# Kernel tuning notes

Measured on AMD Instinct MI355X. Metric: run time of the kernel, lower is better.

Reference implementation:

```python
import jax, jax.numpy as jnp
import numpy as np
from jax import lax

B, H, W, C, K, R, CB = 2, 128, 128, 256, 64, 8, 256


def _conv(x, w, b=None, pad=1, lhs_dil=None, groups=1):
    out = lax.conv_general_dilated(x, w, (1, 1), [(pad, pad), (pad, pad)],
                                   lhs_dilation=lhs_dil, feature_group_count=groups,
                                   dimension_numbers=('NCHW', 'OIHW', 'NCHW'))
    return out if b is None else out + b[None, :, None, None]


def _silu(x):
    return x * jax.nn.sigmoid(x)


def _fuse(l0, l1, l2, p1w, p1b, p2w, p3w):
    # proj1: Conv(k=3)+SiLU (BN folded); proj2/proj3: grouped ConvTranspose2d as lhs-dilated grouped convs
    a = _silu(_conv(l0, p1w, p1b))
    b2 = _conv(l1, p2w, pad=2, lhs_dil=(2, 2), groups=CB)  # ConvT(2CB->CB, k4, s2, p1, g=CB)
    b3 = _conv(l2, p3w, pad=5, lhs_dil=(4, 4), groups=CB)  # ConvT(4CB->CB, k8, s4, p2, g=CB)
    return a + b2 + b3


def _corr_map(emb, trk):
    # emb: [H,W,C], trk: [K,C]; cosine-similarity correlation with local argmax radius masking
    e = emb / jnp.maximum(jnp.linalg.norm(emb, axis=-1, keepdims=True), 1e-12)
    t = trk / jnp.maximum(jnp.linalg.norm(trk, axis=-1, keepdims=True), 1e-12)
    y = jnp.maximum(jnp.einsum('hwc,kc->khw', e, t), 0.0)  # torch.where(y>0, y, 0)
    idx = jnp.argmax(y.reshape(K, -1), axis=1)             # first max, like torch.nonzero(...)[0]
    ai, aj = idx // W, idx % W
    rows = jnp.arange(H)[None, :, None]
    cols = jnp.arange(W)[None, None, :]
    m = ((rows >= (ai[:, None, None] - R)) & (rows < (ai[:, None, None] + R)) &
         (cols >= (aj[:, None, None] - R)) & (cols < (aj[:, None, None] + R)))
    s = jnp.sum(y * m, axis=0)
    return s / jnp.max(s)


def setup_inputs():
    key = jax.random.key(0)
    ks = jax.random.split(key, 32)
    r = lambda i, shp, s=0.02: jax.random.normal(ks[i], shp, jnp.float32) * s
    z = lambda n: jnp.zeros((n,), jnp.float32)
    return dict(
        id_embeding=jax.random.normal(ks[0], (B, H, W, C), jnp.float32),
        tracklets=jax.random.normal(ks[1], (B, K, C), jnp.float32),
        l0=jax.random.normal(ks[2], (B, CB, H, W), jnp.float32),
        l1=jax.random.normal(ks[3], (B, 2 * CB, H // 2, W // 2), jnp.float32),
        l2=jax.random.normal(ks[4], (B, 4 * CB, H // 4, W // 4), jnp.float32),
        b_p1w=r(5, (CB, CB, 3, 3)), b_p1b=z(CB),
        b_p2w=r(6, (CB, 2, 4, 4)), b_p3w=r(7, (CB, 4, 8, 8)),
        b_c1w=r(8, (CB, CB, 3, 3)), b_c1b=z(CB),
        b_c2w=r(9, (4, CB, 3, 3)), b_c2b=z(4),
        h_p1w=r(10, (CB, CB, 3, 3)), h_p1b=z(CB),
        h_p2w=r(11, (CB, 2, 4, 4)), h_p3w=r(12, (CB, 4, 8, 8)),
        h_c1aw=r(13, (CB, 1, 3, 3), 0.1), h_c1ab=z(CB),
        h_c1bw=r(14, (1, CB, 3, 3)), h_c1bb=z(1),
        h_c2aw=r(15, (CB, CB, 3, 3)), h_c2ab=z(CB),
        h_c2bw=r(16, (CB, CB, 3, 3)), h_c2bb=z(CB),
        h_c2cw=r(17, (1, CB, 3, 3)), h_c2cb=z(1),
    )


def reference(id_embeding, tracklets, l0, l1, l2,
              b_p1w, b_p1b, b_p2w, b_p3w, b_c1w, b_c1b, b_c2w, b_c2b,
              h_p1w, h_p1b, h_p2w, h_p3w,
              h_c1aw, h_c1ab, h_c1bw, h_c1bb,
              h_c2aw, h_c2ab, h_c2bw, h_c2bb, h_c2cw, h_c2cb):
    # correlation map per batch -> x_F [B,1,H,W]
    x_F = jax.vmap(_corr_map)(id_embeding, tracklets)[:, None]
    # recheck_Box head
    xd_box = _fuse(l0, l1, l2, b_p1w, b_p1b, b_p2w, b_p3w)
    xb = _silu(_conv(xd_box, b_c1w, b_c1b))
    siambox = jnp.transpose(_conv(xb, b_c2w, b_c2b), (0, 2, 3, 1))  # [B,H,W,4]
    # recheck_heatmap head
    xd_hm = _fuse(l0, l1, l2, h_p1w, h_p1b, h_p2w, h_p3w)
    xf = _conv(_silu(_conv(x_F, h_c1aw, h_c1ab)), h_c1bw, h_c1bb)   # [B,1,H,W]
    t = xf * xd_hm                                                  # broadcast over CB channels
    t = _silu(_conv(t, h_c2aw, h_c2ab))
    t = _silu(_conv(t, h_c2bw, h_c2bb))
    hmmap = jax.nn.sigmoid(_conv(t, h_c2cw, h_c2cb))                # [B,1,H,W]
    return (hmmap, siambox)
```

## Files before the change

kernel.cpp:

```cpp
#include <hip/hip_runtime.h>
#include <math.h>

#define HH 128
#define WW 128
#define HWSZ 16384
#define CC 256
#define KK 64
#define BB 2

typedef __bf16 bf16x8_t __attribute__((ext_vector_type(8)));
typedef float  f32x4_t  __attribute__((ext_vector_type(4)));

__device__ __forceinline__ float silu_f(float v) { return v / (1.f + expf(-v)); }
__device__ __forceinline__ float sigm_f(float v) { return 1.f / (1.f + expf(-v)); }

__device__ __forceinline__ float b2f(unsigned short u) {
    union { unsigned int i; float f; } x; x.i = ((unsigned int)u) << 16; return x.f;
}
__device__ __forceinline__ unsigned short f2b(float f) {
    union { float f; unsigned int i; } x; x.f = f;
    unsigned int r = x.i + 0x7FFFu + ((x.i >> 16) & 1u);
    return (unsigned short)(r >> 16);
}
__device__ __forceinline__ float u2f(unsigned int u) {
    union { unsigned int i; float f; } x; x.i = u; return x.f;
}

__device__ __forceinline__ void cvt_nhwc_body(int bid, float (*T)[128],
                                              const float* __restrict__ in,
                                              unsigned short* __restrict__ out,
                                              unsigned long long* __restrict__ ymax,
                                              unsigned int* __restrict__ umax) {
    const int tid = threadIdx.x;
    if (bid == 0) {
        if (tid < BB * KK) ymax[tid] = 0ull;
        if (tid >= 128 && tid < 128 + BB) umax[tid - 128] = 0u;
    }
    const int y = bid & 127;
    const int b = bid >> 7;
    const float* inb = in + (size_t)b * CC * HWSZ + y * 128;
    unsigned short* outb = out + ((size_t)b * HWSZ + (size_t)y * 128) * CC;

    for (int c0 = 0; c0 < CC; c0 += 32) {
        __syncthreads();
        {
            int cl = tid >> 3;
            int xq = tid & 7;
            const float4* src = (const float4*)(inb + (size_t)(c0 + cl) * HWSZ);
            float4* dst = (float4*)&T[cl][0];
            #pragma unroll
            for (int j = 0; j < 4; j++) dst[xq * 4 + j] = src[xq * 4 + j];
        }
        __syncthreads();
        {
            int x = tid & 127, ch = tid >> 7;
            union { unsigned short u[16]; uint4 v[2]; } pk;
            #pragma unroll
            for (int j = 0; j < 16; j++) pk.u[j] = f2b(T[ch * 16 + j][x]);
            uint4* dst = (uint4*)&outb[(size_t)x * CC + c0 + ch * 16];
            dst[0] = pk.v[0];
            dst[1] = pk.v[1];
        }
    }
}

#define WTSZ (9 * 8 * 256 * 32)
__device__ __forceinline__ void wprep_body(int L,
                                           const float* const* ws,
                                           unsigned short* __restrict__ wtbase) {
    int set = L / 2304;
    int blk = L - set * 2304;
    const float* w = ws[set];
    int idx = blk * 256 + threadIdx.x;
    int e   = idx & 7;
    int co  = (idx >> 3) & 255;
    int g   = (idx >> 11) & 3;
    int v   = idx >> 13;
    int cb  = v / 9;
    int t   = v - cb * 9;
    wtbase[(size_t)set * WTSZ + idx] = f2b(w[((size_t)co * 256 + cb * 32 + g * 8 + e) * 9 + t]);
}

__global__ __launch_bounds__(256) void prep_fused_kernel(
    const float* __restrict__ l0, unsigned short* __restrict__ l0nh,
    unsigned long long* __restrict__ ymax, unsigned int* __restrict__ umax,
    const float* __restrict__ w0, const float* __restrict__ w1,
    const float* __restrict__ w2, const float* __restrict__ w3,
    const float* __restrict__ w4, unsigned short* __restrict__ wtbase)
{
    __shared__ float T[32][128];
    const int bid = blockIdx.x;
    if (bid < 256) {
        cvt_nhwc_body(bid, T, l0, l0nh, ymax, umax);
    } else {
        const float* ws[5] = {w0, w1, w2, w3, w4};
        wprep_body(bid - 256, ws, wtbase);
    }
}

#define EPAD 260
__global__ __launch_bounds__(256) void ycorr_kernel(const float* __restrict__ emb,
                                                    const float* __restrict__ trk,
                                                    float* __restrict__ y,
                                                    unsigned long long* __restrict__ ymax) {
    __shared__ __align__(16) float E[64 * EPAD];
    __shared__ __align__(16) float T[64 * EPAD];
    __shared__ float SE[64];
    __shared__ float ST[64];

    const int tid = threadIdx.x;
    const int b   = blockIdx.y;
    const int hw0 = blockIdx.x * 64;

    const float4* esrc = (const float4*)(emb + ((size_t)b * HWSZ + hw0) * CC);
    #pragma unroll
    for (int i = 0; i < 16; i++) {
        int q  = tid + i * 256;
        int px = q >> 6, c4 = q & 63;
        *(float4*)&E[px * EPAD + c4 * 4] = esrc[(size_t)px * 64 + c4];
    }
    const float4* tsrc = (const float4*)(trk + (size_t)b * KK * CC);
    #pragma unroll
    for (int i = 0; i < 16; i++) {
        int q = tid + i * 256;
        int k = q >> 6, c4 = q & 63;
        *(float4*)&T[k * EPAD + c4 * 4] = tsrc[(size_t)k * 64 + c4];
    }
    __syncthreads();

    if (tid < 64) {
        float ss = 0.f;
        const float4* ep = (const float4*)&E[tid * EPAD];
        #pragma unroll 8
        for (int c4 = 0; c4 < 64; c4++) {
            float4 v = ep[c4];
            ss += v.x * v.x + v.y * v.y + v.z * v.z + v.w * v.w;
        }
        SE[tid] = 1.f / fmaxf(sqrtf(ss), 1e-12f);
    } else if (tid < 128) {
        float ss = 0.f;
        const float4* tp = (const float4*)&T[(tid - 64) * EPAD];
        #pragma unroll 8
        for (int c4 = 0; c4 < 64; c4++) {
            float4 v = tp[c4];
            ss += v.x * v.x + v.y * v.y + v.z * v.z + v.w * v.w;
        }
        ST[tid - 64] = 1.f / fmaxf(sqrtf(ss), 1e-12f);
    }
    __syncthreads();

    const int pg = tid & 15;
    const int kg = tid >> 4;

    float acc[4][4];
    #pragma unroll
    for (int jp = 0; jp < 4; jp++)
        #pragma unroll
        for (int jk = 0; jk < 4; jk++) acc[jp][jk] = 0.f;

    const float* Ep[4];
    const float* Tp[4];
    #pragma unroll
    for (int jp = 0; jp < 4; jp++) Ep[jp] = &E[(jp * 16 + pg) * EPAD];
    #pragma unroll
    for (int jk = 0; jk < 4; jk++) Tp[jk] = &T[(jk * 16 + kg) * EPAD];

    #pragma unroll 2
    for (int c4 = 0; c4 < 64; ++c4) {
        float4 e[4], t[4];
        #pragma unroll
        for (int jp = 0; jp < 4; jp++) e[jp] = *(const float4*)(Ep[jp] + c4 * 4);
        #pragma unroll
        for (int jk = 0; jk < 4; jk++) t[jk] = *(const float4*)(Tp[jk] + c4 * 4);
        #define DOT4(a, t) (fmaf(a.w, t.w, fmaf(a.z, t.z, fmaf(a.y, t.y, a.x * t.x))))
        #pragma unroll
        for (int jp = 0; jp < 4; jp++)
            #pragma unroll
            for (int jk = 0; jk < 4; jk++)
                acc[jp][jk] += DOT4(e[jp], t[jk]);
        #undef DOT4
    }

    #pragma unroll
    for (int jk = 0; jk < 4; jk++) {
        int k = jk * 16 + kg;
        float st = ST[k];
        unsigned long long best = 0ull;
        #pragma unroll
        for (int jp = 0; jp < 4; jp++) {
            int px = jp * 16 + pg;
            float val = fmaxf(acc[jp][jk], 0.f) * SE[px] * st;
            y[((size_t)b * KK + k) * HWSZ + hw0 + px] = val;
            union { float f; unsigned int i; } u; u.f = val;
            unsigned long long pk =
                ((unsigned long long)u.i << 32) | (unsigned)(HWSZ - 1 - (hw0 + px));
            best = best > pk ? best : pk;
        }
        #pragma unroll
        for (int m = 1; m < 16; m <<= 1) {
            unsigned long long o = __shfl_xor(best, m);
            best = best > o ? best : o;
        }
        if (pg == 0) atomicMax(&ymax[b * KK + k], best);
    }
}

__device__ __forceinline__ void smap_body(int bid, char* smem,
                                          const float* __restrict__ y,
                                          const unsigned long long* __restrict__ ymax,
                                          float* __restrict__ s,
                                          unsigned int* __restrict__ umax) {
    int* ai = (int*)smem;
    int* aj = (int*)(smem + 256);
    float* sm = (float*)(smem + 512);

    int b  = bid >> 6;
    int hw = (bid & 63) * 256 + threadIdx.x;
    int h  = hw >> 7, w = hw & 127;
    if (threadIdx.x < KK) {
        unsigned long long p = ymax[b * KK + threadIdx.x];
        int v = HWSZ - 1 - (int)(p & 0xFFFFFFFFull);
        ai[threadIdx.x] = v >> 7;
        aj[threadIdx.x] = v & 127;
    }
    __syncthreads();
    const float* yb = y + (size_t)b * KK * HWSZ;
    float acc = 0.f;
    #pragma unroll 8
    for (int k = 0; k < KK; k++) {
        float v = yb[(size_t)k * HWSZ + hw];
        bool in = (h >= ai[k] - 8) && (h < ai[k] + 8) && (w >= aj[k] - 8) && (w < aj[k] + 8);
        acc += in ? v : 0.f;
    }
    s[(size_t)b * HWSZ + hw] = acc;

    sm[threadIdx.x] = acc;
    __syncthreads();
    for (int st = 128; st > 0; st >>= 1) {
        if (threadIdx.x < st) sm[threadIdx.x] = fmaxf(sm[threadIdx.x], sm[threadIdx.x + st]);
        __syncthreads();
    }
    if (threadIdx.x == 0) {
        union { float f; unsigned int i; } x; x.f = sm[0];
        atomicMax(&umax[b], x.i);
    }
}

template <int HEADS>
__device__ __forceinline__ void deconv_body(int bid, char* smem,
                                            const float* __restrict__ l1,
                                            const float* __restrict__ l2,
                                            const float* __restrict__ w2a,
                                            const float* __restrict__ w3a,
                                            const float* __restrict__ w2b,
                                            const float* __restrict__ w3b,
                                            unsigned short* __restrict__ outA,
                                            unsigned short* __restrict__ outB) {
    float (*L1)[64][64] = (float (*)[64][64])smem;
    float (*L2)[32][32] = (float (*)[32][32])(smem + 32768);

    const int tid = threadIdx.x;
    const int g   = bid & 255;
    const int b   = bid >> 8;

    const float4* l1b = (const float4*)(l1 + ((size_t)b * 2 * CC + 2 * g) * 4096);
    float4* L1p = (float4*)&L1[0][0][0];
    #pragma unroll
    for (int i = 0; i < 8; i++) L1p[tid + i * 256] = l1b[tid + i * 256];
    const float4* l2b = (const float4*)(l2 + ((size_t)b * 4 * CC + 4 * g) * 1024);
    float4* L2p = (float4*)&L2[0][0][0];
    #pragma unroll
    for (int i = 0; i < 4; i++) L2p[tid + i * 256] = l2b[tid + i * 256];

    const int x    = tid & 127;
    const int ytop = tid >> 7;

    const int pxo = x & 1, pyo = ytop & 1;
    const int mx0 = (x + pxo - 2) >> 1;
    const int dy2 = (ytop + pyo - 2) >> 1;
    const bool nok0 = (unsigned)mx0 < 64u;
    const bool nok1 = (unsigned)(mx0 + 1) < 64u;
    const int nc0 = mx0 & 63, nc1 = (mx0 + 1) & 63;

    const int px3 = (5 - (x & 3)) & 3;
    const int n30 = (x + px3 - 5) >> 2;
    const bool n3ok0 = (unsigned)n30 < 32u;
    const bool n3ok1 = (unsigned)(n30 + 1) < 32u;
    const int n3c0 = n30 & 31, n3c1 = (n30 + 1) & 31;
    int dy3[2], py3v[2];
    #pragma unroll
    for (int ph = 0; ph < 2; ph++) {
        int py3 = (5 - ((ytop + 2 * ph) & 3)) & 3;
        py3v[ph] = py3;
        dy3[ph] = (2 * ph + ytop + py3 - 5) >> 2;
    }

    __syncthreads();

    const float* w2s[2] = {w2a, w2b};
    const float* w3s[2] = {w3a, w3b};
    unsigned short* outs[2] = {outA, outB};

    #pragma unroll 1
    for (int hd = 0; hd < HEADS; ++hd) {
        const float* w2g = w2s[hd] + (size_t)g * 32;
        const float* w3g = w3s[hd] + (size_t)g * 256;

        float W2[2][2][2];
        #pragma unroll
        for (int ci = 0; ci < 2; ci++)
            #pragma unroll
            for (int a = 0; a < 2; a++)
                #pragma unroll
                for (int c = 0; c < 2; c++)
                    W2[ci][a][c] = w2g[ci * 16 + (pyo + 2 * a) * 4 + (pxo + 2 * c)];
        float W3[2][4][2][2];
        #pragma unroll
        for (int ph = 0; ph < 2; ph++)
            #pragma unroll
            for (int ci = 0; ci < 4; ci++)
                #pragma unroll
                for (int a = 0; a < 2; a++)
                    #pragma unroll
                    for (int c = 0; c < 2; c++)
                        W3[ph][ci][a][c] = w3g[ci * 64 + (py3v[ph] + 4 * a) * 8 + (px3 + 4 * c)];

        unsigned short* outb = outs[hd] + ((size_t)b * CC + g) * HWSZ;

        #pragma unroll 2
        for (int ii = 0; ii < 32; ++ii) {
            #pragma unroll
            for (int ph = 0; ph < 2; ph++) {
                const int i = 2 * ii + ph;
                float acc = 0.f;
                {
                    const int m0 = i + dy2;
                    #pragma unroll
                    for (int a = 0; a < 2; a++) {
                        int m = m0 + a;
                        bool mok = (unsigned)m < 64u;
                        int mc = m & 63;
                        #pragma unroll
                        for (int ci = 0; ci < 2; ci++) {
                            float v0 = (mok && nok0) ? L1[ci][mc][nc0] : 0.f;
                            float v1 = (mok && nok1) ? L1[ci][mc][nc1] : 0.f;
                            acc = fmaf(W2[ci][a][0], v0, acc);
                            acc = fmaf(W2[ci][a][1], v1, acc);
                        }
                    }
                }
                {
                    const int m0 = ii + dy3[ph];
                    #pragma unroll
                    for (int a = 0; a < 2; a++) {
                        int m = m0 + a;
                        bool mok = (unsigned)m < 32u;
                        int mc = m & 31;
                        #pragma unroll
                        for (int ci = 0; ci < 4; ci++) {
                            float v0 = (mok && n3ok0) ? L2[ci][mc][n3c0] : 0.f;
                            float v1 = (mok && n3ok1) ? L2[ci][mc][n3c1] : 0.f;
                            acc = fmaf(W3[ph][ci][a][0], v0, acc);
                            acc = fmaf(W3[ph][ci][a][1], v1, acc);
                        }
                    }
                }
                outb[(size_t)i * 256 + tid] = f2b(acc);
            }
        }
    }
}

__global__ __launch_bounds__(256) void smap_kernel(const float* __restrict__ y,
                                                   const unsigned long long* __restrict__ ymax,
                                                   float* __restrict__ s,
                                                   unsigned int* __restrict__ umax) {
    __shared__ __align__(16) char smem[1536];
    smap_body(blockIdx.x, smem, y, ymax, s, umax);
}
template <int HEADS>
__global__ __launch_bounds__(256) void deconv_kernel(const float* __restrict__ l1,
                                                     const float* __restrict__ l2,
                                                     const float* __restrict__ w2a,
                                                     const float* __restrict__ w3a,
                                                     const float* __restrict__ w2b,
                                                     const float* __restrict__ w3b,
                                                     unsigned short* __restrict__ outA,
                                                     unsigned short* __restrict__ outB) {
    __shared__ __align__(16) char smem[49152];
    deconv_body<HEADS>(blockIdx.x, smem, l1, l2, w2a, w3a, w2b, w3b, outA, outB);
}

__global__ __launch_bounds__(256) void smapdeconv_kernel(
    const float* __restrict__ y, const unsigned long long* __restrict__ ymax,
    float* __restrict__ s, unsigned int* __restrict__ umax,
    const float* __restrict__ l1, const float* __restrict__ l2,
    const float* __restrict__ w2a, const float* __restrict__ w3a,
    const float* __restrict__ w2b, const float* __restrict__ w3b,
    unsigned short* __restrict__ outA, unsigned short* __restrict__ outB)
{
    __shared__ __align__(16) char smem[49152];
    const int bid = blockIdx.x;
    if (bid < 128) smap_body(bid, smem, y, ymax, s, umax);
    else           deconv_body<2>(bid - 128, smem, l1, l2, w2a, w3a, w2b, w3b, outA, outB);
}

template <int ADDB, int MULF>
__device__ __forceinline__ void conv_mfma_body(
    int y0, int co0, int b,
    const unsigned short* __restrict__ in,
    const unsigned short* __restrict__ wt,
    const float* __restrict__ bias,
    const unsigned short* __restrict__ addb,
    const float* __restrict__ xf,
    unsigned short* __restrict__ out,
    unsigned short (*Alds)[3 * 130 * 32])
{
    const int tid  = threadIdx.x;
    const int lane = tid & 63;
    const int wv   = tid >> 6;
    const int wco  = wv >> 1;
    const int wpx  = wv & 1;
    const int l15  = lane & 15;
    const int kg   = lane >> 4;

    const unsigned short* inb = in + (size_t)b * HWSZ * CC;
    const float* xfb = MULF ? (xf + (size_t)b * HWSZ) : nullptr;
    const unsigned short* wp = wt + (size_t)kg * 2048 + (size_t)(co0 + wco * 64 + l15) * 8;

    int ach[3][4];
    #pragma unroll
    for (int tl = 0; tl < 3; tl++)
        #pragma unroll
        for (int f = 0; f < 4; f++) {
            int px = wpx * 64 + f * 16 + l15 + tl;
            ach[tl][f] = (px * 4 + (kg ^ ((px >> 1) & 3))) * 8;
        }

    f32x4_t acc[4][4];
    #pragma unroll
    for (int i = 0; i < 4; i++)
        #pragma unroll
        for (int j = 0; j < 4; j++)
            acc[i][j] = (f32x4_t){0.f, 0.f, 0.f, 0.f};

    if (tid < 48) {
        int q4 = tid & 3;
        int hp = (tid >> 2) & 1;
        int r  = (tid >> 3) % 3;
        int bi = tid / 24;
        int px = hp ? 129 : 0;
        int chunk = (r * 130 + px) * 4 + (q4 ^ ((px >> 1) & 3));
        *reinterpret_cast<uint4*>(&Alds[bi][chunk * 8]) = make_uint4(0u, 0u, 0u, 0u);
    }

    uint4 streg[6];
    float sxf[6];

    auto load_A = [&](int cb) {
        #pragma unroll
        for (int i = 0; i < 6; i++) {
            int q   = tid + i * 256;
            int q4  = q & 3;
            int pxi = (q >> 2) & 127;
            int r   = q >> 9;
            int gy  = y0 - 1 + r;
            uint4 v = make_uint4(0u, 0u, 0u, 0u);
            float fxv = 0.f;
            if ((unsigned)gy < 128u) {
                v = *reinterpret_cast<const uint4*>(
                        inb + ((size_t)(gy * 128 + pxi)) * CC + cb * 32 + q4 * 8);
                if (MULF) fxv = xfb[gy * 128 + pxi];
            }
            streg[i] = v;
            if (MULF) sxf[i] = fxv;
        }
    };
    auto write_A = [&](int bufi) {
        #pragma unroll
        for (int i = 0; i < 6; i++) {
            int q   = tid + i * 256;
            int q4  = q & 3;
            int pxi = (q >> 2) & 127;
            int r   = q >> 9;
            int px  = pxi + 1;
            int chunk = (r * 130 + px) * 4 + (q4 ^ ((px >> 1) & 3));
            uint4 v = streg[i];
            if (MULF) {
                union { unsigned short u[8]; uint4 w; } pk;
                pk.w = v;
                float fm = sxf[i];
                #pragma unroll
                for (int e = 0; e < 8; e++) pk.u[e] = f2b(b2f(pk.u[e]) * fm);
                v = pk.w;
            }
            *reinterpret_cast<uint4*>(&Alds[bufi][chunk * 8]) = v;
        }
    };

    load_A(0);
    write_A(0);

    bf16x8_t W[3][4], P[2][4];
    #pragma unroll
    for (int f = 0; f < 4; f++) W[0][f] = *reinterpret_cast<const bf16x8_t*>(wp + f * 128);
    #pragma unroll
    for (int f = 0; f < 4; f++) W[1][f] = *reinterpret_cast<const bf16x8_t*>(wp + 8192 + f * 128);

    __syncthreads();
    #pragma unroll
    for (int f = 0; f < 4; f++)
        P[0][f] = *reinterpret_cast<const bf16x8_t*>(&Alds[0][ach[0][f]]);

    for (int cb = 0; cb < 8; ++cb) {
        const int bufi = cb & 1;
        if (cb + 1 < 8) load_A(cb + 1);
        const unsigned short* wcb = wp + (size_t)cb * 73728;
        #pragma unroll
        for (int t = 0; t < 9; ++t) {
            if (cb < 7 || t < 7) {
                #pragma unroll
                for (int f = 0; f < 4; f++)
                    W[(t + 2) % 3][f] = *reinterpret_cast<const bf16x8_t*>(
                        wcb + (t + 2) * 8192 + f * 128);
            }
            if (t < 8) {
                const int aoff = ((t + 1) / 3) * 4160;
                #pragma unroll
                for (int f = 0; f < 4; f++)
                    P[(t + 1) & 1][f] = *reinterpret_cast<const bf16x8_t*>(
                        &Alds[bufi][aoff + ach[(t + 1) % 3][f]]);
            }
            __builtin_amdgcn_sched_barrier(0);
            #pragma unroll
            for (int cf = 0; cf < 4; cf++)
                #pragma unroll
                for (int pf = 0; pf < 4; pf++)
                    acc[cf][pf] = __builtin_amdgcn_mfma_f32_16x16x32_bf16(
                        W[t % 3][cf], P[t & 1][pf], acc[cf][pf], 0, 0, 0);
        }
        if (cb + 1 < 8) write_A(bufi ^ 1);
        __syncthreads();
        if (cb + 1 < 8) {
            #pragma unroll
            for (int f = 0; f < 4; f++)
                P[0][f] = *reinterpret_cast<const bf16x8_t*>(&Alds[(cb + 1) & 1][ach[0][f]]);
        }
    }

    size_t outB = ((size_t)b * HWSZ + (size_t)y0 * 128) * CC;
    #pragma unroll
    for (int cf = 0; cf < 4; cf++) {
        int co = co0 + wco * 64 + cf * 16 + kg * 4;
        float bs0 = bias[co], bs1 = bias[co + 1], bs2 = bias[co + 2], bs3 = bias[co + 3];
        #pragma unroll
        for (int pf = 0; pf < 4; pf++) {
            int x = wpx * 64 + pf * 16 + l15;
            float v0 = silu_f(acc[cf][pf][0] + bs0);
            float v1 = silu_f(acc[cf][pf][1] + bs1);
            float v2 = silu_f(acc[cf][pf][2] + bs2);
            float v3 = silu_f(acc[cf][pf][3] + bs3);
            if (ADDB) {
                size_t ab = ((size_t)b * CC + co) * HWSZ + (size_t)y0 * 128 + x;
                v0 += b2f(addb[ab]);
                v1 += b2f(addb[ab + HWSZ]);
                v2 += b2f(addb[ab + 2 * HWSZ]);
                v3 += b2f(addb[ab + 3 * HWSZ]);
            }
            union { unsigned short u[4]; uint2 v; } pk;
            pk.u[0] = f2b(v0); pk.u[1] = f2b(v1); pk.u[2] = f2b(v2); pk.u[3] = f2b(v3);
            *reinterpret_cast<uint2*>(&out[outB + (size_t)x * CC + co]) = pk.v;
        }
    }
}

template <int ADDB, int MULF>
__global__ __launch_bounds__(256, 2) void conv_mfma_kernel(
    const unsigned short* __restrict__ in,
    const unsigned short* __restrict__ wt,
    const float* __restrict__ bias,
    const unsigned short* __restrict__ addb,
    const float* __restrict__ xf,
    unsigned short* __restrict__ out)
{
    __shared__ __align__(16) unsigned short Alds[2][3 * 130 * 32];
    const int l   = (blockIdx.x & 7) * 64 + (blockIdx.x >> 3);
    const int y0  = l >> 2;
    const int co0 = ((l >> 1) & 1) * 128;
    const int b   = l & 1;
    conv_mfma_body<ADDB, MULF>(y0, co0, b, in, wt, bias, addb, xf, out, Alds);
}

__global__ __launch_bounds__(256, 2) void conv_mfma_dual_kernel(
    const unsigned short* __restrict__ in,
    const unsigned short* __restrict__ wt2set,
    const float* __restrict__ biasB,
    const float* __restrict__ biasH,
    const unsigned short* __restrict__ addbB,
    const unsigned short* __restrict__ addbH,
    unsigned short* __restrict__ outB,
    unsigned short* __restrict__ outH)
{
    __shared__ __align__(16) unsigned short Alds[2][3 * 130 * 32];
    const int l    = (blockIdx.x & 7) * 128 + (blockIdx.x >> 3);
    const int y0   = l >> 3;
    const int c3   = l & 7;
    const int head = c3 >> 2;
    const int co0  = ((c3 >> 1) & 1) * 128;
    const int b    = c3 & 1;
    conv_mfma_body<1, 0>(y0, co0, b, in, wt2set + (size_t)head * WTSZ,
                         head ? biasH : biasB, head ? addbH : addbB,
                         nullptr, head ? outH : outB, Alds);
}

__global__ __launch_bounds__(256, 2) void conv_mfma_dualmix_kernel(
    const unsigned short* __restrict__ in0,
    const unsigned short* __restrict__ in1,
    const unsigned short* __restrict__ wt0,
    const unsigned short* __restrict__ wt1,
    const float* __restrict__ bias0,
    const float* __restrict__ bias1,
    const float* __restrict__ xf,
    unsigned short* __restrict__ out0,
    unsigned short* __restrict__ out1)
{
    __shared__ __align__(16) unsigned short Alds[2][3 * 130 * 32];
    const int l    = (blockIdx.x & 7) * 128 + (blockIdx.x >> 3);
    const int y0   = l >> 3;
    const int c3   = l & 7;
    const int head = c3 >> 2;
    const int co0  = ((c3 >> 1) & 1) * 128;
    const int b    = c3 & 1;
    if (head == 0)
        conv_mfma_body<0, 0>(y0, co0, b, in0, wt0, bias0, nullptr, nullptr, out0, Alds);
    else
        conv_mfma_body<0, 1>(y0, co0, b, in1, wt1, bias1, nullptr, xf, out1, Alds);
}

__global__ __launch_bounds__(256) void conv_c1a_kernel(const float* __restrict__ s,
                                                       const unsigned int* __restrict__ umax,
                                                       const float* __restrict__ w,
                                                       const float* __restrict__ bias,
                                                       unsigned short* __restrict__ out) {
    __shared__ float W[2304];
    __shared__ float S[3][34];

    const int tid = threadIdx.x;
    const int idx = blockIdx.x;
    const int b   = idx >> 9;
    const int seg = idx & 511;
    const int y   = seg >> 2;
    const int x0  = (seg & 3) * 32;

    for (int i = tid; i < 2304; i += 256) W[i] = w[i];
    if (tid < 102) {
        int r = tid / 34, xx = tid - r * 34;
        int gy = y - 1 + r, gx = x0 - 1 + xx;
        S[r][xx] = ((unsigned)gy < 128u && (unsigned)gx < 128u)
                       ? s[(size_t)b * HWSZ + gy * 128 + gx] : 0.f;
    }
    __syncthreads();

    const float im = 1.f / u2f(umax[b]);
    const int cog = tid >> 5;
    const int px  = tid & 31;

    float sv[9];
    #pragma unroll
    for (int r = 0; r < 3; r++)
        #pragma unroll
        for (int d = 0; d < 3; d++)
            sv[r * 3 + d] = S[r][px + d];

    unsigned short* op =
        &out[((size_t)b * HWSZ + (size_t)y * 128 + x0 + px) * CC + cog * 32];
    #pragma unroll
    for (int q = 0; q < 4; q++) {
        union { unsigned short u[8]; uint4 v; } pk;
        #pragma unroll
        for (int j = 0; j < 8; j++) {
            int co = cog * 32 + q * 8 + j;
            float a = 0.f;
            #pragma unroll
            for (int t = 0; t < 9; t++) a = fmaf(W[co * 9 + t], sv[t], a);
            pk.u[j] = f2b(silu_f(a * im + bias[co]));
        }
        *reinterpret_cast<uint4*>(op + q * 8) = pk.v;
    }
}

template <int COUT, int MODE>
__device__ __forceinline__ void small_conv_body(int bid, float* WL,
                                                const unsigned short* __restrict__ in,
                                                const float* __restrict__ w,
                                                const float* __restrict__ bias,
                                                float* __restrict__ out)
{
    const int tid = threadIdx.x;
    for (int i = tid; i < COUT * 2304; i += 256) {
        int e = i & 7;
        int g = (i >> 3) & 31;
        int rest = i >> 8;
        int t = rest % 9;
        int co = rest / 9;
        WL[((co * 9 + t) * 32 + g) * 12 + e] = w[((size_t)co * 256 + g * 8 + e) * 9 + t];
    }
    __syncthreads();

    const int lane = tid & 63;
    const int wv   = tid >> 6;
    const int c32  = lane & 31;
    const int ps   = lane >> 5;
    const int grp  = bid * 4 + wv;
    const int base = grp * 4;
    const int b    = base >> 14;
    const int pix  = base & (HWSZ - 1);
    const int y    = pix >> 7;
    const int x0   = pix & 127;
    const int p0x  = x0 + 2 * ps;

    const unsigned short* inb = in + (size_t)b * HWSZ * CC;

    uint4 d[3][4];
    #pragma unroll
    for (int r = 0; r < 3; r++) {
        int gy = y - 1 + r;
        #pragma unroll
        for (int cx = 0; cx < 4; cx++) {
            int gx = p0x - 1 + cx;
            uint4 v = make_uint4(0u, 0u, 0u, 0u);
            if ((unsigned)gy < 128u && (unsigned)gx < 128u)
                v = *reinterpret_cast<const uint4*>(
                        inb + ((size_t)(gy * 128 + gx)) * CC + c32 * 8);
            d[r][cx] = v;
        }
    }

    float acc[2][COUT];
    #pragma unroll
    for (int p = 0; p < 2; p++)
        #pragma unroll
        for (int c = 0; c < COUT; c++) acc[p][c] = 0.f;

    #pragma unroll
    for (int r = 0; r < 3; r++) {
        float f[4][8];
        #pragma unroll
        for (int cx = 0; cx < 4; cx++) {
            union { unsigned short u[8]; uint4 v; } pk;
            pk.v = d[r][cx];
            #pragma unroll
            for (int e = 0; e < 8; e++) f[cx][e] = b2f(pk.u[e]);
        }
        #pragma unroll
        for (int dx = 0; dx < 3; dx++) {
            #pragma unroll
            for (int co = 0; co < COUT; co++) {
                int bse = ((co * 9 + r * 3 + dx) * 32 + c32) * 12;
                float4 wa = *(const float4*)&WL[bse];
                float4 wb = *(const float4*)&WL[bse + 4];
                #pragma unroll
                for (int p = 0; p < 2; p++) {
                    const float* ff = f[dx + p];
                    float a = acc[p][co];
                    a = fmaf(ff[0], wa.x, a); a = fmaf(ff[1], wa.y, a);
                    a = fmaf(ff[2], wa.z, a); a = fmaf(ff[3], wa.w, a);
                    a = fmaf(ff[4], wb.x, a); a = fmaf(ff[5], wb.y, a);
                    a = fmaf(ff[6], wb.z, a); a = fmaf(ff[7], wb.w, a);
                    acc[p][co] = a;
                }
            }
        }
    }

    #pragma unroll
    for (int m = 1; m <= 16; m <<= 1)
        #pragma unroll
        for (int p = 0; p < 2; p++)
            #pragma unroll
            for (int co = 0; co < COUT; co++)
                acc[p][co] += __shfl_xor(acc[p][co], m);

    if (c32 == 0) {
        #pragma unroll
        for (int p = 0; p < 2; p++) {
            size_t pixidx = (size_t)base + 2 * ps + p;
            if (MODE == 0) {
                ((float4*)out)[pixidx] = make_float4(
                    acc[p][0] + bias[0],
                    acc[p][COUT > 1 ? 1 : 0] + bias[COUT > 1 ? 1 : 0],
                    acc[p][COUT > 2 ? 2 : 0] + bias[COUT > 2 ? 2 : 0],
                    acc[p][COUT > 3 ? 3 : 0] + bias[COUT > 3 ? 3 : 0]);
            } else if (MODE == 1) {
                out[pixidx] = acc[p][0] + bias[0];
            } else {
                out[pixidx] = sigm_f(acc[p][0] + bias[0]);
            }
        }
    }
}

template <int COUT, int MODE>
__global__ __launch_bounds__(256) void small_conv_kernel(
    const unsigned short* __restrict__ in,
    const float* __restrict__ w,
    const float* __restrict__ bias,
    float* __restrict__ out)
{
    __shared__ float WL[COUT * 9 * 32 * 12];
    small_conv_body<COUT, MODE>(blockIdx.x, WL, in, w, bias, out);
}

__global__ __launch_bounds__(256, 2) void t3c2_kernel(
    const unsigned short* __restrict__ t2in,
    const unsigned short* __restrict__ wt4,
    const float* __restrict__ biasT3,
    unsigned short* __restrict__ t3out,
    const unsigned short* __restrict__ xbin,
    const float* __restrict__ c2w,
    const float* __restrict__ c2b,
    float* __restrict__ boxout)
{
    __shared__ __align__(16) char smem[55296];
    const int bid = blockIdx.x;
    if (bid < 512) {
        const int l   = (bid & 7) * 64 + (bid >> 3);
        const int y0  = l >> 2;
        const int co0 = ((l >> 1) & 1) * 128;
        const int b   = l & 1;
        conv_mfma_body<0, 0>(y0, co0, b, t2in, wt4, biasT3, nullptr, nullptr, t3out,
                             (unsigned short (*)[3 * 130 * 32])smem);
    } else {
        small_conv_body<4, 0>(bid - 512, (float*)smem, xbin, c2w, c2b, boxout);
    }
}

extern "C" void kernel_launch(void* const* d_in, const int* in_sizes, int n_in,
                              void* d_out, int out_size, void* d_ws, size_t ws_size,
                              hipStream_t stream) {
    const float* emb    = (const float*)d_in[0];
    const float* trk    = (const float*)d_in[1];
    const float* l0     = (const float*)d_in[2];
    const float* l1     = (const float*)d_in[3];
    const float* l2     = (const float*)d_in[4];
    const float* b_p1w  = (const float*)d_in[5];
    const float* b_p1b  = (const float*)d_in[6];
    const float* b_p2w  = (const float*)d_in[7];
    const float* b_p3w  = (const float*)d_in[8];
    const float* b_c1w  = (const float*)d_in[9];
    const float* b_c1b  = (const float*)d_in[10];
    const float* b_c2w  = (const float*)d_in[11];
    const float* b_c2b  = (const float*)d_in[12];
    const float* h_p1w  = (const float*)d_in[13];
    const float* h_p1b  = (const float*)d_in[14];
    const float* h_p2w  = (const float*)d_in[15];
    const float* h_p3w  = (const float*)d_in[16];
    const float* h_c1aw = (const float*)d_in[17];
    const float* h_c1ab = (const float*)d_in[18];
    const float* h_c1bw = (const float*)d_in[19];
    const float* h_c1bb = (const float*)d_in[20];
    const float* h_c2aw = (const float*)d_in[21];
    const float* h_c2ab = (const float*)d_in[22];
    const float* h_c2bw = (const float*)d_in[23];
    const float* h_c2bb = (const float*)d_in[24];
    const float* h_c2cw = (const float*)d_in[25];
    const float* h_c2cb = (const float*)d_in[26];

    float* outp = (float*)d_out;

    const size_t ACT = (size_t)BB * CC * HWSZ;
    const size_t WT  = (size_t)WTSZ;
    const size_t SMALLS = 132096;

    unsigned short* l0nh = (unsigned short*)d_ws;
    unsigned short* wtP  = l0nh + ACT;
    unsigned short* bufA = wtP + 5 * WT;
    unsigned short* bufB = bufA + ACT;
    unsigned short* bufC = bufB + ACT;
    float* sbuf   = (float*)(bufC + ACT);
    float* xfb    = sbuf + (size_t)BB * HWSZ;
    unsigned long long* ymax = (unsigned long long*)(xfb + (size_t)BB * HWSZ);
    unsigned int* umax = (unsigned int*)(ymax + BB * KK);
    unsigned short* bufD = bufC + ACT + SMALLS;
    float* ybuf   = (float*)bufB;

    const size_t NEED = (size_t)(bufD + ACT - l0nh) * sizeof(unsigned short);
    const bool fast = ws_size >= NEED;

    prep_fused_kernel<<<256 + 11520, 256, 0, stream>>>(
        l0, l0nh, ymax, umax, b_p1w, h_p1w, b_c1w, h_c2aw, h_c2bw, wtP);

    ycorr_kernel<<<dim3(256, BB), 256, 0, stream>>>(emb, trk, ybuf, ymax);

    if (fast) {
        smapdeconv_kernel<<<128 + 512, 256, 0, stream>>>(
            ybuf, ymax, sbuf, umax,
            l1, l2, b_p2w, b_p3w, h_p2w, h_p3w, bufA, bufD);
        conv_c1a_kernel<<<1024, 256, 0, stream>>>(sbuf, umax, h_c1aw, h_c1ab, bufB);
        small_conv_kernel<1, 1><<<2048, 256, 0, stream>>>(bufB, h_c1bw, h_c1bb, xfb);
        conv_mfma_dual_kernel<<<1024, 256, 0, stream>>>(l0nh, wtP, b_p1b, h_p1b,
                                                        bufA, bufD, bufB, bufC);
        conv_mfma_dualmix_kernel<<<1024, 256, 0, stream>>>(bufB, bufC,
                                                           wtP + 2 * WT, wtP + 3 * WT,
                                                           b_c1b, h_c2ab, xfb,
                                                           bufD, bufA);
        t3c2_kernel<<<512 + 2048, 256, 0, stream>>>(bufA, wtP + 4 * WT, h_c2bb, bufB,
                                                    bufD, b_c2w, b_c2b,
                                                    outp + BB * HWSZ);
        small_conv_kernel<1, 2><<<2048, 256, 0, stream>>>(bufB, h_c2cw, h_c2cb, outp);
    } else {
        smap_kernel<<<64 * BB, 256, 0, stream>>>(ybuf, ymax, sbuf, umax);
        deconv_kernel<1><<<BB * CC, 256, 0, stream>>>(l1, l2, b_p2w, b_p3w,
                                                      nullptr, nullptr, bufA, nullptr);
        conv_mfma_kernel<1, 0><<<512, 256, 0, stream>>>(l0nh, wtP, b_p1b, bufA,
                                                        nullptr, bufB);
        conv_mfma_kernel<0, 0><<<512, 256, 0, stream>>>(bufB, wtP + 2 * WT, b_c1b,
                                                        nullptr, nullptr, bufC);
        small_conv_kernel<4, 0><<<2048, 256, 0, stream>>>(bufC, b_c2w, b_c2b,
                                                          outp + BB * HWSZ);
        deconv_kernel<1><<<BB * CC, 256, 0, stream>>>(l1, l2, h_p2w, h_p3w,
                                                      nullptr, nullptr, bufA, nullptr);
        conv_mfma_kernel<1, 0><<<512, 256, 0, stream>>>(l0nh, wtP + 1 * WT, h_p1b, bufA,
                                                        nullptr, bufB);
        conv_c1a_kernel<<<1024, 256, 0, stream>>>(sbuf, umax, h_c1aw, h_c1ab, bufC);
        small_conv_kernel<1, 1><<<2048, 256, 0, stream>>>(bufC, h_c1bw, h_c1bb, xfb);
        conv_mfma_kernel<0, 1><<<512, 256, 0, stream>>>(bufB, wtP + 3 * WT, h_c2ab,
                                                        nullptr, xfb, bufA);
        conv_mfma_kernel<0, 0><<<512, 256, 0, stream>>>(bufA, wtP + 4 * WT, h_c2bb,
                                                        nullptr, nullptr, bufC);
        small_conv_kernel<1, 2><<<2048, 256, 0, stream>>>(bufC, h_c2cw, h_c2cb, outp);
    }
}
```

Measured before the change: 376.0 us.

## Fuse heatmap c1a/c1b small convs into dual proj1 MFMA kernel launch

Replaces the separate conv_c1a and small_conv launches with a per-row t1xf body that computes the 1->256 conv, SiLU and 256->1 conv entirely in shared memory. It then appends those blocks to the dual proj1 MFMA conv launch, so they run as extra blocks alongside it. This removes two kernel launches and the 256-channel intermediate that went through global memory. In exchange, the scalar 2D recompute runs on only 128 of 256 threads, and the fused blocks share the launch-bounds and shared-memory footprint of the MFMA kernel.

```diff
diff --git a/kernel.cpp b/kernel.cpp
--- a/kernel.cpp
+++ b/kernel.cpp
@@ -405,6 +405,80 @@
     else           deconv_body<2>(bid - 128, smem, l1, l2, w2a, w3a, w2b, w3b, outA, outB);
 }
 
+__device__ __forceinline__ void t1xf_body(int bid, char* smemc,
+                                          const float* __restrict__ s,
+                                          const unsigned int* __restrict__ umax,
+                                          const float* __restrict__ w1a,
+                                          const float* __restrict__ b1a,
+                                          const float* __restrict__ w1b,
+                                          const float* __restrict__ b1b,
+                                          float* __restrict__ xf)
+{
+    float* WA = (float*)smemc;
+    float* BA = WA + 2304;
+    float* WB = BA + 256;
+    float* S  = WB + 2304;
+    float* T1 = S + 660;
+
+    const int tid = threadIdx.x;
+    const int b = bid >> 7;
+    const int y = bid & 127;
+
+    for (int i = tid; i < 2304; i += 256) WA[i] = w1a[i];
+    for (int i = tid; i < 2304; i += 256) WB[i] = w1b[i];
+    BA[tid] = b1a[tid];
+
+    const float* sb = s + (size_t)b * HWSZ;
+    for (int i = tid; i < 660; i += 256) {
+        int r = i / 132, cc = i - r * 132;
+        int gy = y - 2 + r, gx = cc - 2;
+        S[i] = ((unsigned)gy < 128u && (unsigned)gx < 128u) ? sb[gy * 128 + gx] : 0.f;
+    }
+    __syncthreads();
+    const float im = 1.f / u2f(umax[b]);
+
+    float acc = 0.f;
+    for (int c0 = 0; c0 < 256; c0 += 8) {
+        for (int i = tid; i < 8 * 390; i += 256) {
+            int ch  = i / 390;
+            int rem = i - ch * 390;
+            int rr  = rem / 130;
+            int cc  = rem - rr * 130;
+            int r   = y - 1 + rr;
+            int cg  = cc - 1;
+            float v = 0.f;
+            if ((unsigned)r < 128u && (unsigned)cg < 128u) {
+                const float* wc = &WA[(c0 + ch) * 9];
+                float a = 0.f;
+                #pragma unroll
+                for (int dy = 0; dy < 3; dy++)
+                    #pragma unroll
+                    for (int dx = 0; dx < 3; dx++)
+                        a = fmaf(wc[dy * 3 + dx], S[(rr + dy) * 132 + cc + dx], a);
+                v = silu_f(a * im + BA[c0 + ch]);
+            }
+            T1[i] = v;
+        }
+        __syncthreads();
+        if (tid < 128) {
+            int x = tid;
+            #pragma unroll
+            for (int ch = 0; ch < 8; ch++) {
+                const float* wc = &WB[(c0 + ch) * 9];
+                const float* t  = &T1[ch * 390];
+                #pragma unroll
+                for (int dy = 0; dy < 3; dy++) {
+                    acc = fmaf(wc[dy * 3 + 0], t[dy * 130 + x], acc);
+                    acc = fmaf(wc[dy * 3 + 1], t[dy * 130 + x + 1], acc);
+                    acc = fmaf(wc[dy * 3 + 2], t[dy * 130 + x + 2], acc);
+                }
+            }
+        }
+        __syncthreads();
+    }
+    if (tid < 128) xf[(size_t)b * HWSZ + (size_t)y * 128 + tid] = acc + b1b[0];
+}
+
 template <int ADDB, int MULF>
 __device__ __forceinline__ void conv_mfma_body(
     int y0, int co0, int b,
@@ -589,6 +663,41 @@
     const int co0 = ((l >> 1) & 1) * 128;
     const int b   = l & 1;
     conv_mfma_body<ADDB, MULF>(y0, co0, b, in, wt, bias, addb, xf, out, Alds);
+}
+
+__global__ __launch_bounds__(256, 2) void dualp1_t1xf_kernel(
+    const unsigned short* __restrict__ in,
+    const unsigned short* __restrict__ wt2set,
+    const float* __restrict__ biasB,
+    const float* __restrict__ biasH,
+    const unsigned short* __restrict__ addbB,
+    const unsigned short* __restrict__ addbH,
+    unsigned short* __restrict__ outB,
+    unsigned short* __restrict__ outH,
+    const float* __restrict__ s,
+    const unsigned int* __restrict__ umax,
+    const float* __restrict__ w1a,
+    const float* __restrict__ b1a,
+    const float* __restrict__ w1b,
+    const float* __restrict__ b1b,
+    float* __restrict__ xf)
+{
+    __shared__ __align__(16) char smem[2 * 3 * 130 * 32 * 2];
+    const int bid = blockIdx.x;
+    if (bid < 1024) {
+        const int l    = (bid & 7) * 128 + (bid >> 3);
+        const int y0   = l >> 3;
+        const int c3   = l & 7;
+        const int head = c3 >> 2;
+        const int co0  = ((c3 >> 1) & 1) * 128;
+        const int b    = c3 & 1;
+        conv_mfma_body<1, 0>(y0, co0, b, in, wt2set + (size_t)head * WTSZ,
+                             head ? biasH : biasB, head ? addbH : addbB,
+                             nullptr, head ? outH : outB,
+                             (unsigned short (*)[3 * 130 * 32])smem);
+    } else {
+        t1xf_body(bid - 1024, smem, s, umax, w1a, b1a, w1b, b1b, xf);
+    }
 }
 
 __global__ __launch_bounds__(256, 2) void conv_mfma_dual_kernel(
@@ -896,10 +1005,9 @@
         smapdeconv_kernel<<<128 + 512, 256, 0, stream>>>(
             ybuf, ymax, sbuf, umax,
             l1, l2, b_p2w, b_p3w, h_p2w, h_p3w, bufA, bufD);
-        conv_c1a_kernel<<<1024, 256, 0, stream>>>(sbuf, umax, h_c1aw, h_c1ab, bufB);
-        small_conv_kernel<1, 1><<<2048, 256, 0, stream>>>(bufB, h_c1bw, h_c1bb, xfb);
-        conv_mfma_dual_kernel<<<1024, 256, 0, stream>>>(l0nh, wtP, b_p1b, h_p1b,
-                                                        bufA, bufD, bufB, bufC);
+        dualp1_t1xf_kernel<<<1024 + 256, 256, 0, stream>>>(
+            l0nh, wtP, b_p1b, h_p1b, bufA, bufD, bufB, bufC,
+            sbuf, umax, h_c1aw, h_c1ab, h_c1bw, h_c1bb, xfb);
         conv_mfma_dualmix_kernel<<<1024, 256, 0, stream>>>(bufB, bufC,
                                                            wtP + 2 * WT, wtP + 3 * WT,
                                                            b_c1b, h_c2ab, xfb,
```

Result: slower. 459.4 us (+22.2%).
